# Kernel tuning notes

Hardware: AMD Instinct MI355X
Metric: run time of the kernel (lower is better)

The kernel has to match this reference:

```python
import jax, jax.numpy as jnp
import numpy as np

B, L, DM = 4, 409, 192            # batch, tokens (1 cls + 16 target + 196 template + 196 search), d_model
DI, DS, DR, K, DEPTH = 384, 16, 12, 4, 24   # d_inner=2*DM, d_state, dt_rank=ceil(DM/16), d_conv, depth
EPS = 1e-5


def setup_inputs() -> dict:
    key = jax.random.key(0)
    ks = list(jax.random.split(key, 16))
    def rn(i, shape, s=0.02):
        return jax.random.normal(ks[i], shape, jnp.float32) * s
    # S4D-real init: A = [1..d_state] per channel, stored as log
    A_log = jnp.log(jnp.tile(jnp.arange(1, DS + 1, dtype=jnp.float32), (DEPTH, DI, 1)))
    return {
        "tokens": jax.random.normal(ks[0], (B, L, DM), jnp.float32),
        "norm_w": jnp.ones((DEPTH, DM), jnp.float32),
        "in_proj_w": rn(1, (DEPTH, 2 * DI, DM)),
        "conv_w": rn(2, (DEPTH, DI, 1, K), 0.2),
        "conv_b": jnp.zeros((DEPTH, DI), jnp.float32),
        "conv_w_b": rn(3, (DEPTH, DI, 1, K), 0.2),
        "conv_b_b": jnp.zeros((DEPTH, DI), jnp.float32),
        "x_proj_w": rn(4, (DEPTH, DR + 2 * DS, DI)),
        "x_proj_w_b": rn(5, (DEPTH, DR + 2 * DS, DI)),
        "dt_proj_w": rn(6, (DEPTH, DI, DR), 0.1),
        "dt_bias": rn(7, (DEPTH, DI), 0.5),
        "dt_proj_w_b": rn(8, (DEPTH, DI, DR), 0.1),
        "dt_bias_b": rn(9, (DEPTH, DI), 0.5),
        "A_log": A_log,
        "A_log_b": A_log,
        "D_param": jnp.ones((DEPTH, DI), jnp.float32),
        "D_param_b": jnp.ones((DEPTH, DI), jnp.float32),
        "out_proj_w": rn(10, (DEPTH, DM, DI)),
        "norm_f_w": jnp.ones((DM,), jnp.float32),
    }


def _rms(x, w):
    return x * jax.lax.rsqrt(jnp.mean(x * x, -1, keepdims=True) + EPS) * w


def _causal_conv(x, w, b):
    # x [B,L,DI]; depthwise causal conv1d, kernel K (pad left K-1)
    y = jax.lax.conv_general_dilated(
        jnp.swapaxes(x, 1, 2), w, (1,), [(K - 1, 0)],
        dimension_numbers=("NCH", "OIH", "NCH"), feature_group_count=DI)
    return jnp.swapaxes(y + b[None, :, None], 1, 2)


def _selective_scan(u, delta, A, Bm, Cm, Dp):
    # u,delta [B,L,DI]; A [DI,DS]; Bm,Cm [B,L,DS]; Dp [DI]
    def step(h, inp):
        u_t, d_t, b_t, c_t = inp  # [B,DI],[B,DI],[B,DS],[B,DS]
        h = h * jnp.exp(d_t[..., None] * A) + (d_t * u_t)[..., None] * b_t[:, None, :]
        return h, jnp.einsum("bdn,bn->bd", h, c_t)
    h0 = jnp.zeros((u.shape[0], A.shape[0], A.shape[1]), u.dtype)
    xs = tuple(jnp.swapaxes(t, 0, 1) for t in (u, delta, Bm, Cm))
    _, ys = jax.lax.scan(step, h0, xs)
    return jnp.swapaxes(ys, 0, 1) + u * Dp


def _scan_dir(xin, cw, cb, xpw, dtw, dtb, a_log, dp):
    xf = jax.nn.silu(_causal_conv(xin, cw, cb))
    x_dbl = jnp.einsum("bld,ed->ble", xf, xpw)
    dt, Bm, Cm = jnp.split(x_dbl, [DR, DR + DS], axis=-1)
    dt = jax.nn.softplus(jnp.einsum("blr,dr->bld", dt, dtw) + dtb)
    return _selective_scan(xf, dt, -jnp.exp(a_log), Bm, Cm, dp)


def _mixer(x, p):
    # bimamba v2: forward scan + backward (flipped) scan with separate params
    xz = jnp.einsum("bld,ed->ble", x, p["in_proj_w"])
    xin, z = jnp.split(xz, 2, axis=-1)
    y_f = _scan_dir(xin, p["conv_w"], p["conv_b"], p["x_proj_w"],
                    p["dt_proj_w"], p["dt_bias"], p["A_log"], p["D_param"])
    y_b = _scan_dir(xin[:, ::-1], p["conv_w_b"], p["conv_b_b"], p["x_proj_w_b"],
                    p["dt_proj_w_b"], p["dt_bias_b"], p["A_log_b"], p["D_param_b"])[:, ::-1]
    y = (y_f + y_b) * jax.nn.silu(z) * 0.5   # z-gating + if_divide_out
    return jnp.einsum("ble,de->bld", y, p["out_proj_w"])


def reference(tokens, norm_w, in_proj_w, conv_w, conv_b, conv_w_b, conv_b_b,
              x_proj_w, x_proj_w_b, dt_proj_w, dt_bias, dt_proj_w_b, dt_bias_b,
              A_log, A_log_b, D_param, D_param_b, out_proj_w, norm_f_w):
    stacked = {"norm_w": norm_w, "in_proj_w": in_proj_w,
               "conv_w": conv_w, "conv_b": conv_b, "conv_w_b": conv_w_b, "conv_b_b": conv_b_b,
               "x_proj_w": x_proj_w, "x_proj_w_b": x_proj_w_b,
               "dt_proj_w": dt_proj_w, "dt_bias": dt_bias,
               "dt_proj_w_b": dt_proj_w_b, "dt_bias_b": dt_bias_b,
               "A_log": A_log, "A_log_b": A_log_b,
               "D_param": D_param, "D_param_b": D_param_b,
               "out_proj_w": out_proj_w}

    def layer(carry, p):
        hidden, residual = carry
        residual = residual + hidden          # add (first layer: residual starts at 0)
        h = _rms(residual, p["norm_w"])       # fused_add_norm prenorm path (RMSNorm)
        h = _mixer(h, p)
        return (h, residual), None

    init = (tokens, jnp.zeros_like(tokens))
    (hidden, residual), _ = jax.lax.scan(layer, init, stacked)
    return _rms(residual + hidden, norm_f_w)
```

## Files before the change

kernel.cpp:

```cpp
#include <hip/hip_runtime.h>
#include <math.h>

#define BB     4
#define LLEN   409
#define DMODEL 192
#define DINNER 384
#define DSTATE 16
#define DRANK  12
#define KCONV  4
#define NLAYER 24
#define NROW   (BB*LLEN)
#define EPSF   1e-5f
#define CH2    16
#define NCH2   26

__device__ __forceinline__ float siluf(float x){ return x/(1.f+__expf(-x)); }
__device__ __forceinline__ float softplusf(float x){ return (x>20.f)? x : log1pf(__expf(x)); }

__global__ void k_prep(const float* __restrict__ tokens, float* __restrict__ residual,
    const float* __restrict__ alF, const float* __restrict__ alB,
    float* __restrict__ anF, float* __restrict__ anB){
  int i = blockIdx.x*256+threadIdx.x;
  if (i < NROW*DMODEL) residual[i] = tokens[i];
  if (i < NLAYER*DINNER*DSTATE){
    int l = i/(DINNER*DSTATE); int rem = i%(DINNER*DSTATE);
    int nn = rem/DINNER, d = rem%DINNER;
    size_t src = ((size_t)l*DINNER + d)*DSTATE + nn;
    anF[i] = -expf(alF[src]);
    anB[i] = -expf(alB[src]);
  }
}

__global__ __launch_bounds__(256) void k_txp(const float* __restrict__ src,
    float* __restrict__ dst, int R, int C, int RP){
  __shared__ float t[32][33];
  int l = blockIdx.z;
  int c0 = blockIdx.x*32, r0 = blockIdx.y*32;
  const float* s = src + (size_t)l*R*C;
  float* d = dst + (size_t)l*C*RP;
  int tx = threadIdx.x, ty = threadIdx.y;
  #pragma unroll
  for (int yy=ty; yy<32; yy+=8){
    int rr = r0+yy, cc = c0+tx;
    t[yy][tx] = (rr<R && cc<C)? s[(size_t)rr*C+cc] : 0.f;
  }
  __syncthreads();
  #pragma unroll
  for (int yy=ty; yy<32; yy+=8){
    int cc = c0+yy, rr = r0+tx;
    if (cc<C && rr<RP) d[(size_t)cc*RP+rr] = t[tx][yy];
  }
}

__global__ __launch_bounds__(256) void k_prenorm(const float* __restrict__ residual,
    const float* __restrict__ norm_w, float* __restrict__ xn){
  int wv = threadIdx.x>>6, lane = threadIdx.x&63;
  int row = blockIdx.x*4 + wv;
  if (row >= NROW) return;
  float v[3]; float s = 0.f;
  #pragma unroll
  for (int q=0;q<3;q++){ v[q] = residual[(size_t)row*DMODEL + lane + q*64]; s += v[q]*v[q]; }
  #pragma unroll
  for (int off=1; off<64; off<<=1) s += __shfl_xor(s, off, 64);
  float sc = rsqrtf(s/(float)DMODEL + EPSF);
  #pragma unroll
  for (int q=0;q<3;q++) xn[(size_t)row*DMODEL + lane + q*64] = v[q]*sc*norm_w[lane + q*64];
}

__global__ __launch_bounds__(256) void k_gemm_in(const float* __restrict__ xn,
    const float* __restrict__ Wt, float* __restrict__ xz){
  __shared__ __align__(16) float w_lds[192*64];
  __shared__ __align__(16) float a_lds[192*20];
  int tid = threadIdx.x, r0 = blockIdx.x*16, c0 = blockIdx.y*64;
  {
    int j4 = (tid&15)*4, kr = tid>>4;
    #pragma unroll
    for (int s=0;s<12;s++){
      int k = kr + s*16;
      *reinterpret_cast<float4*>(&w_lds[k*64+j4]) =
        *reinterpret_cast<const float4*>(&Wt[(size_t)k*768 + c0 + j4]);
    }
  }
  {
    int i = tid>>4, kc = (tid&15)*12;
    int row = r0+i;
    #pragma unroll
    for (int m=0;m<12;m+=4){
      float4 v = make_float4(0.f,0.f,0.f,0.f);
      if (row<NROW) v = *reinterpret_cast<const float4*>(&xn[(size_t)row*192 + kc + m]);
      a_lds[(kc+m+0)*20+i]=v.x; a_lds[(kc+m+1)*20+i]=v.y;
      a_lds[(kc+m+2)*20+i]=v.z; a_lds[(kc+m+3)*20+i]=v.w;
    }
  }
  __syncthreads();
  int j = tid & 63, rg = tid >> 6;
  float acc[4] = {0.f,0.f,0.f,0.f};
  #pragma unroll 8
  for (int k=0;k<192;k++){
    float w = w_lds[k*64+j];
    float4 a = *reinterpret_cast<const float4*>(&a_lds[k*20 + rg*4]);
    acc[0]+=a.x*w; acc[1]+=a.y*w; acc[2]+=a.z*w; acc[3]+=a.w*w;
  }
  #pragma unroll
  for (int q=0;q<4;q++){
    int row = r0 + rg*4 + q;
    if (row<NROW) xz[(size_t)row*768 + c0 + j] = acc[q];
  }
}

__global__ __launch_bounds__(256) void k_conv(const float* __restrict__ xz,
    const float* __restrict__ cwf, const float* __restrict__ cbf,
    const float* __restrict__ cwb, const float* __restrict__ cbb,
    float* __restrict__ xf_f, float* __restrict__ xf_b){
  int idx = blockIdx.x*256 + threadIdx.x;
  if (idx >= NROW*(DINNER/4)) return;
  int d4 = (idx % (DINNER/4))*4; int bl = idx / (DINNER/4);
  int b = bl / LLEN; int l = bl % LLEN;
  int dir = blockIdx.y;
  const float* cw = dir? cwb : cwf;
  const float* cb = dir? cbb : cbf;
  float4 w0 = *reinterpret_cast<const float4*>(&cw[(d4+0)*KCONV]);
  float4 w1 = *reinterpret_cast<const float4*>(&cw[(d4+1)*KCONV]);
  float4 w2 = *reinterpret_cast<const float4*>(&cw[(d4+2)*KCONV]);
  float4 w3 = *reinterpret_cast<const float4*>(&cw[(d4+3)*KCONV]);
  float4 acc = *reinterpret_cast<const float4*>(&cb[d4]);
  const float* wa0 = (const float*)&w0; const float* wa1 = (const float*)&w1;
  const float* wa2 = (const float*)&w2; const float* wa3 = (const float*)&w3;
  #pragma unroll
  for (int k=0;k<KCONV;k++){
    int o = dir? (LLEN-1-l-k+3) : (l-3+k);
    bool ok = dir? (l+k>=3) : (o>=0);
    if (ok){
      float4 x = *reinterpret_cast<const float4*>(&xz[((size_t)(b*LLEN+o))*768 + d4]);
      acc.x += wa0[k]*x.x; acc.y += wa1[k]*x.y; acc.z += wa2[k]*x.z; acc.w += wa3[k]*x.w;
    }
  }
  float* out = dir? xf_b : xf_f;
  float4 r; r.x = siluf(acc.x); r.y = siluf(acc.y); r.z = siluf(acc.z); r.w = siluf(acc.w);
  *reinterpret_cast<float4*>(&out[(size_t)bl*DINNER + d4]) = r;
}

__global__ __launch_bounds__(256) void k_xp2(
    const float* __restrict__ xf_f, const float* __restrict__ xf_b,
    const float* __restrict__ WxpPF, const float* __restrict__ WxpPB,
    const float* __restrict__ WdtF, const float* __restrict__ WdtB,
    const float* __restrict__ dtbF, const float* __restrict__ dtbB,
    float* __restrict__ dtbc_f, float* __restrict__ dtbc_b,
    float* __restrict__ dt_f, float* __restrict__ dt_b){
  __shared__ __align__(16) float w_lds[192*64];
  __shared__ __align__(16) float a_lds[192*20];
  __shared__ float dtin_s[16*12];
  int dir = blockIdx.z;
  const float* xf  = dir? xf_b : xf_f;
  const float* Wxp = dir? WxpPB : WxpPF;
  const float* Wdt = dir? WdtB : WdtF;
  const float* dtb = dir? dtbB : dtbF;
  float* dtbc = dir? dtbc_b : dtbc_f;
  float* dtp  = dir? dt_b  : dt_f;
  int tid = threadIdx.x, r0 = blockIdx.x*16;
  int j = tid & 63, rg = tid >> 6;
  float acc[4] = {0.f,0.f,0.f,0.f};
  for (int c=0;c<2;c++){
    int K0 = c*192;
    if (c) __syncthreads();
    {
      int j4 = (tid&15)*4, kr = tid>>4;
      #pragma unroll
      for (int s=0;s<12;s++){
        int k = kr + s*16;
        *reinterpret_cast<float4*>(&w_lds[k*64+j4]) =
          *reinterpret_cast<const float4*>(&Wxp[(size_t)(K0+k)*64 + j4]);
      }
    }
    {
      int i = tid>>4, kc = (tid&15)*12;
      int row = r0+i;
      #pragma unroll
      for (int m=0;m<12;m+=4){
        float4 v = make_float4(0.f,0.f,0.f,0.f);
        if (row<NROW) v = *reinterpret_cast<const float4*>(&xf[(size_t)row*DINNER + K0 + kc + m]);
        a_lds[(kc+m+0)*20+i]=v.x; a_lds[(kc+m+1)*20+i]=v.y;
        a_lds[(kc+m+2)*20+i]=v.z; a_lds[(kc+m+3)*20+i]=v.w;
      }
    }
    __syncthreads();
    #pragma unroll 8
    for (int k=0;k<192;k++){
      float w = w_lds[k*64+j];
      float4 a = *reinterpret_cast<const float4*>(&a_lds[k*20 + rg*4]);
      acc[0]+=a.x*w; acc[1]+=a.y*w; acc[2]+=a.z*w; acc[3]+=a.w*w;
    }
  }
  __syncthreads();
  #pragma unroll
  for (int q=0;q<4;q++){
    int i = rg*4+q, row = r0+i;
    if (j<44 && row<NROW) dtbc[(size_t)row*44 + j] = acc[q];
    if (j<12) dtin_s[i*12 + j] = acc[q];
  }
  __syncthreads();
  for (int idx=tid; idx<12*DINNER; idx+=256) w_lds[idx] = Wdt[idx];
  __syncthreads();
  for (int idx=tid; idx<16*DINNER; idx+=256){
    int i = idx/DINNER, dd = idx - i*DINNER;
    int row = r0+i;
    float v = dtb[dd];
    #pragma unroll
    for (int r=0;r<12;r++) v += dtin_s[i*12+r]*w_lds[r*DINNER+dd];
    if (row<NROW) dtp[(size_t)row*DINNER+dd] = softplusf(v);
  }
}

__global__ __launch_bounds__(128) void k_scan1(
    const float* __restrict__ xf_f, const float* __restrict__ xf_b,
    const float* __restrict__ dtbc_f, const float* __restrict__ dtbc_b,
    const float* __restrict__ dt_f, const float* __restrict__ dt_b,
    const float* __restrict__ anF, const float* __restrict__ anB,
    float* __restrict__ q_buf, float* __restrict__ sdt_buf){
  int dir = blockIdx.z;
  int b  = blockIdx.y / NCH2;
  int ch = blockIdx.y % NCH2;
  if (ch == NCH2-1) return;
  const float* xf   = dir? xf_b  : xf_f;
  const float* dtbc = dir? dtbc_b: dtbc_f;
  const float* dtp  = dir? dt_b  : dt_f;
  const float* an   = dir? anB   : anF;
  int t0 = ch*CH2;
  int T  = CH2;
  int d0 = blockIdx.x*128;
  size_t base = (size_t)b*LLEN + t0;
  __shared__ float dt_s[CH2*128], u_s[CH2*128];
  __shared__ __align__(16) float B_s[CH2*16];
  int tid = threadIdx.x;
  for (int t=0;t<T;t++){
    dt_s[t*128+tid] = dtp[(base+t)*DINNER + d0 + tid];
    u_s [t*128+tid] = xf [(base+t)*DINNER + d0 + tid];
  }
  for (int idx = tid; idx < T*16; idx += 128){
    int t = idx>>4, n = idx&15;
    B_s[idx] = dtbc[(base+t)*44 + 12 + n];
  }
  __syncthreads();
  int d = d0 + tid;
  float A[16], h[16];
  #pragma unroll
  for (int n=0;n<16;n++){ A[n] = an[n*DINNER + d]; h[n] = 0.f; }
  float sdt = 0.f;
  for (int t=0;t<T;t++){
    float dtv = dt_s[t*128+tid];
    float du  = dtv * u_s[t*128+tid];
    float Bv[16];
    #pragma unroll
    for (int q=0;q<4;q++) *reinterpret_cast<float4*>(&Bv[q*4]) =
        *reinterpret_cast<const float4*>(&B_s[t*16 + q*4]);
    #pragma unroll
    for (int n=0;n<16;n++) h[n] = h[n]*__expf(dtv*A[n]) + du*Bv[n];
    sdt += dtv;
  }
  size_t ci = ((size_t)dir*BB + b)*NCH2 + ch;
  float* qo = &q_buf[(ci*DINNER + d)*DSTATE];
  #pragma unroll
  for (int q=0;q<4;q++) *reinterpret_cast<float4*>(&qo[q*4]) =
      make_float4(h[q*4+0], h[q*4+1], h[q*4+2], h[q*4+3]);
  sdt_buf[ci*DINNER + d] = sdt;
}

__global__ __launch_bounds__(128) void k_scan2(
    const float* __restrict__ xf_f, const float* __restrict__ xf_b,
    const float* __restrict__ dtbc_f, const float* __restrict__ dtbc_b,
    const float* __restrict__ dt_f, const float* __restrict__ dt_b,
    const float* __restrict__ anF, const float* __restrict__ anB,
    const float* __restrict__ DpF, const float* __restrict__ DpB,
    const float* __restrict__ q_buf, const float* __restrict__ sdt_buf,
    float* __restrict__ y_fo, float* __restrict__ y_bo){
  int dir = blockIdx.z;
  int b  = blockIdx.y / NCH2;
  int ch = blockIdx.y % NCH2;
  const float* xf   = dir? xf_b  : xf_f;
  const float* dtbc = dir? dtbc_b: dtbc_f;
  const float* dtp  = dir? dt_b  : dt_f;
  const float* an   = dir? anB   : anF;
  const float* Dp   = dir? DpB   : DpF;
  float* y = dir? y_bo : y_fo;
  int t0 = ch*CH2;
  int T  = (t0+CH2<=LLEN)? CH2 : (LLEN-t0);
  int d0 = blockIdx.x*128;
  size_t base = (size_t)b*LLEN + t0;
  __shared__ float dt_s[CH2*128], u_s[CH2*128];
  __shared__ __align__(16) float B_s[CH2*16], C_s[CH2*16];
  int tid = threadIdx.x;
  for (int t=0;t<T;t++){
    dt_s[t*128+tid] = dtp[(base+t)*DINNER + d0 + tid];
    u_s [t*128+tid] = xf [(base+t)*DINNER + d0 + tid];
  }
  for (int idx = tid; idx < T*16; idx += 128){
    int t = idx>>4, n = idx&15;
    B_s[idx] = dtbc[(base+t)*44 + 12 + n];
    C_s[idx] = dtbc[(base+t)*44 + 28 + n];
  }
  __syncthreads();
  int d = d0 + tid;
  float A[16], h[16];
  #pragma unroll
  for (int n=0;n<16;n++){ A[n] = an[n*DINNER + d]; h[n] = 0.f; }
  size_t sbase = ((size_t)dir*BB + b)*NCH2;
  for (int cc=0; cc<ch; cc++){
    float sv = sdt_buf[(sbase+cc)*DINNER + d];
    const float* qp = &q_buf[((sbase+cc)*DINNER + d)*DSTATE];
    float qv[16];
    #pragma unroll
    for (int q=0;q<4;q++) *reinterpret_cast<float4*>(&qv[q*4]) =
        *reinterpret_cast<const float4*>(&qp[q*4]);
    #pragma unroll
    for (int n=0;n<16;n++) h[n] = qv[n] + __expf(A[n]*sv)*h[n];
  }
  float Dd = Dp[d];
  for (int t=0;t<T;t++){
    float dtv = dt_s[t*128+tid];
    float u   = u_s [t*128+tid];
    float du  = dtv*u;
    float Bv[16], Cv[16];
    #pragma unroll
    for (int q=0;q<4;q++){
      *reinterpret_cast<float4*>(&Bv[q*4]) = *reinterpret_cast<const float4*>(&B_s[t*16+q*4]);
      *reinterpret_cast<float4*>(&Cv[q*4]) = *reinterpret_cast<const float4*>(&C_s[t*16+q*4]);
    }
    float y0=0.f, y1=0.f, y2=0.f, y3=0.f;
    #pragma unroll
    for (int n=0;n<16;n+=4){
      h[n+0] = h[n+0]*__expf(dtv*A[n+0]) + du*Bv[n+0];
      h[n+1] = h[n+1]*__expf(dtv*A[n+1]) + du*Bv[n+1];
      h[n+2] = h[n+2]*__expf(dtv*A[n+2]) + du*Bv[n+2];
      h[n+3] = h[n+3]*__expf(dtv*A[n+3]) + du*Bv[n+3];
      y0 += h[n+0]*Cv[n+0]; y1 += h[n+1]*Cv[n+1];
      y2 += h[n+2]*Cv[n+2]; y3 += h[n+3]*Cv[n+3];
    }
    y[(base+t)*DINNER + d] = (y0+y1)+(y2+y3) + u*Dd;
  }
}

__global__ __launch_bounds__(256) void k_gate(
    const float* __restrict__ y_f, const float* __restrict__ y_b,
    const float* __restrict__ xz, float* __restrict__ g){
  int idx = blockIdx.x*256 + threadIdx.x;
  if (idx >= NROW*(DINNER/4)) return;
  int d4 = (idx % (DINNER/4))*4; int row = idx / (DINNER/4);
  int b = row/LLEN, l = row%LLEN;
  int rrow = b*LLEN + (LLEN-1-l);
  float4 yf = *reinterpret_cast<const float4*>(&y_f[(size_t)row*DINNER + d4]);
  float4 yb = *reinterpret_cast<const float4*>(&y_b[(size_t)rrow*DINNER + d4]);
  float4 z  = *reinterpret_cast<const float4*>(&xz[(size_t)row*768 + DINNER + d4]);
  float4 r;
  r.x = (yf.x+yb.x)*siluf(z.x)*0.5f; r.y = (yf.y+yb.y)*siluf(z.y)*0.5f;
  r.z = (yf.z+yb.z)*siluf(z.z)*0.5f; r.w = (yf.w+yb.w)*siluf(z.w)*0.5f;
  *reinterpret_cast<float4*>(&g[(size_t)row*DINNER + d4]) = r;
}

__global__ __launch_bounds__(256) void k_gemm_out(const float* __restrict__ g,
    const float* __restrict__ Wt, float* __restrict__ residual){
  __shared__ __align__(16) float w_lds[192*64];
  __shared__ __align__(16) float a_lds[192*20];
  int tid = threadIdx.x, r0 = blockIdx.x*16, c0 = blockIdx.y*64;
  int j = tid & 63, rg = tid >> 6;
  float acc[4] = {0.f,0.f,0.f,0.f};
  for (int c=0;c<2;c++){
    int K0 = c*192;
    if (c) __syncthreads();
    {
      int j4 = (tid&15)*4, kr = tid>>4;
      #pragma unroll
      for (int s=0;s<12;s++){
        int k = kr + s*16;
        *reinterpret_cast<float4*>(&w_lds[k*64+j4]) =
          *reinterpret_cast<const float4*>(&Wt[(size_t)(K0+k)*192 + c0 + j4]);
      }
    }
    {
      int i = tid>>4, kc = (tid&15)*12;
      int row = r0+i;
      #pragma unroll
      for (int m=0;m<12;m+=4){
        float4 v = make_float4(0.f,0.f,0.f,0.f);
        if (row<NROW) v = *reinterpret_cast<const float4*>(&g[(size_t)row*DINNER + K0 + kc + m]);
        a_lds[(kc+m+0)*20+i]=v.x; a_lds[(kc+m+1)*20+i]=v.y;
        a_lds[(kc+m+2)*20+i]=v.z; a_lds[(kc+m+3)*20+i]=v.w;
      }
    }
    __syncthreads();
    #pragma unroll 8
    for (int k=0;k<192;k++){
      float w = w_lds[k*64+j];
      float4 a = *reinterpret_cast<const float4*>(&a_lds[k*20 + rg*4]);
      acc[0]+=a.x*w; acc[1]+=a.y*w; acc[2]+=a.z*w; acc[3]+=a.w*w;
    }
  }
  #pragma unroll
  for (int q=0;q<4;q++){
    int row = r0 + rg*4 + q;
    if (row<NROW) residual[(size_t)row*DMODEL + c0 + j] += acc[q];
  }
}

__global__ __launch_bounds__(256) void k_final(const float* __restrict__ residual,
    const float* __restrict__ nfw, float* __restrict__ out){
  int wv = threadIdx.x>>6, lane = threadIdx.x&63;
  int row = blockIdx.x*4 + wv;
  if (row >= NROW) return;
  float v[3]; float s = 0.f;
  #pragma unroll
  for (int q=0;q<3;q++){ v[q] = residual[(size_t)row*DMODEL + lane + q*64]; s += v[q]*v[q]; }
  #pragma unroll
  for (int off=1; off<64; off<<=1) s += __shfl_xor(s, off, 64);
  float sc = rsqrtf(s/(float)DMODEL + EPSF);
  #pragma unroll
  for (int q=0;q<3;q++) out[(size_t)row*DMODEL + lane + q*64] = v[q]*sc*nfw[lane + q*64];
}

extern "C" void kernel_launch(void* const* d_in, const int* in_sizes, int n_in,
                              void* d_out, int out_size, void* d_ws, size_t ws_size,
                              hipStream_t stream){
  const float* tokens     = (const float*)d_in[0];
  const float* norm_w     = (const float*)d_in[1];
  const float* in_proj_w  = (const float*)d_in[2];
  const float* conv_w     = (const float*)d_in[3];
  const float* conv_b     = (const float*)d_in[4];
  const float* conv_w_b   = (const float*)d_in[5];
  const float* conv_b_b   = (const float*)d_in[6];
  const float* x_proj_w   = (const float*)d_in[7];
  const float* x_proj_w_b = (const float*)d_in[8];
  const float* dt_proj_w  = (const float*)d_in[9];
  const float* dt_bias    = (const float*)d_in[10];
  const float* dt_proj_w_b= (const float*)d_in[11];
  const float* dt_bias_b  = (const float*)d_in[12];
  const float* A_log      = (const float*)d_in[13];
  const float* A_log_b    = (const float*)d_in[14];
  const float* D_param    = (const float*)d_in[15];
  const float* D_param_b  = (const float*)d_in[16];
  const float* out_proj_w = (const float*)d_in[17];
  const float* norm_f_w   = (const float*)d_in[18];

  float* ws = (float*)d_ws;
  size_t off = 0;
  float* residual = ws + off; off += (size_t)NROW*DMODEL;
  float* xn       = ws + off; off += (size_t)NROW*DMODEL;
  float* xz       = ws + off; off += (size_t)NROW*768;
  float* xf_f     = ws + off; off += (size_t)NROW*DINNER;
  float* xf_b     = ws + off; off += (size_t)NROW*DINNER;
  float* dtbc_f   = ws + off; off += (size_t)NROW*44;
  float* dtbc_b   = ws + off; off += (size_t)NROW*44;
  float* dt_f     = ws + off; off += (size_t)NROW*DINNER;
  float* dt_b     = ws + off; off += (size_t)NROW*DINNER;
  float* y_f      = ws + off; off += (size_t)NROW*DINNER;
  float* y_b      = ws + off; off += (size_t)NROW*DINNER;
  float* gbuf     = ws + off; off += (size_t)NROW*DINNER;
  float* q_buf    = ws + off; off += (size_t)2*BB*NCH2*DINNER*DSTATE;
  float* sdt_buf  = ws + off; off += (size_t)2*BB*NCH2*DINNER;
  float* WtIn     = ws + off; off += (size_t)NLAYER*DMODEL*768;
  float* WtXpPF   = ws + off; off += (size_t)NLAYER*DINNER*64;
  float* WtXpPB   = ws + off; off += (size_t)NLAYER*DINNER*64;
  float* WtDtF    = ws + off; off += (size_t)NLAYER*DRANK*DINNER;
  float* WtDtB    = ws + off; off += (size_t)NLAYER*DRANK*DINNER;
  float* WtOut    = ws + off; off += (size_t)NLAYER*DINNER*DMODEL;
  float* AnTF     = ws + off; off += (size_t)NLAYER*DINNER*DSTATE;
  float* AnTB     = ws + off; off += (size_t)NLAYER*DINNER*DSTATE;
  if (off*sizeof(float) > ws_size) return;

  k_prep<<<dim3((NROW*DMODEL+255)/256),256,0,stream>>>(tokens, residual, A_log, A_log_b, AnTF, AnTB);
  dim3 tb(32,8);
  k_txp<<<dim3(6,24,NLAYER),tb,0,stream>>>(in_proj_w,  WtIn,   768, 192, 768);
  k_txp<<<dim3(12,2,NLAYER),tb,0,stream>>>(x_proj_w,   WtXpPF,  44, 384,  64);
  k_txp<<<dim3(12,2,NLAYER),tb,0,stream>>>(x_proj_w_b, WtXpPB,  44, 384,  64);
  k_txp<<<dim3(1,12,NLAYER),tb,0,stream>>>(dt_proj_w,  WtDtF,  384,  12, 384);
  k_txp<<<dim3(1,12,NLAYER),tb,0,stream>>>(dt_proj_w_b,WtDtB,  384,  12, 384);
  k_txp<<<dim3(12,6,NLAYER),tb,0,stream>>>(out_proj_w, WtOut,  192, 384, 192);

  const int RT16 = (NROW+15)/16;
  const int EW4  = (NROW*(DINNER/4)+255)/256;
  for (int l=0; l<NLAYER; l++){
    k_prenorm<<<dim3((NROW+3)/4),256,0,stream>>>(residual, norm_w + (size_t)l*DMODEL, xn);
    k_gemm_in<<<dim3(RT16,12),256,0,stream>>>(xn, WtIn + (size_t)l*DMODEL*768, xz);
    k_conv<<<dim3(EW4,2),256,0,stream>>>(xz,
        conv_w + (size_t)l*DINNER*KCONV, conv_b + (size_t)l*DINNER,
        conv_w_b + (size_t)l*DINNER*KCONV, conv_b_b + (size_t)l*DINNER, xf_f, xf_b);
    k_xp2<<<dim3(RT16,1,2),256,0,stream>>>(xf_f, xf_b,
        WtXpPF + (size_t)l*DINNER*64, WtXpPB + (size_t)l*DINNER*64,
        WtDtF + (size_t)l*DRANK*DINNER, WtDtB + (size_t)l*DRANK*DINNER,
        dt_bias + (size_t)l*DINNER, dt_bias_b + (size_t)l*DINNER,
        dtbc_f, dtbc_b, dt_f, dt_b);
    k_scan1<<<dim3(3,BB*NCH2,2),128,0,stream>>>(xf_f, xf_b, dtbc_f, dtbc_b, dt_f, dt_b,
        AnTF + (size_t)l*DINNER*DSTATE, AnTB + (size_t)l*DINNER*DSTATE, q_buf, sdt_buf);
    k_scan2<<<dim3(3,BB*NCH2,2),128,0,stream>>>(xf_f, xf_b, dtbc_f, dtbc_b, dt_f, dt_b,
        AnTF + (size_t)l*DINNER*DSTATE, AnTB + (size_t)l*DINNER*DSTATE,
        D_param + (size_t)l*DINNER, D_param_b + (size_t)l*DINNER,
        q_buf, sdt_buf, y_f, y_b);
    k_gate<<<dim3(EW4),256,0,stream>>>(y_f, y_b, xz, gbuf);
    k_gemm_out<<<dim3(RT16,3),256,0,stream>>>(gbuf, WtOut + (size_t)l*DINNER*DMODEL, residual);
  }
  k_final<<<dim3((NROW+3)/4),256,0,stream>>>(residual, norm_f_w, (float*)d_out);
}
```

Measured before the change: 2.388 ms.

## Fuse forward/backward scan pass-2 with gating into one kernel

The second scan pass now handles both directions in one block. The block scans the forward chunk, keeps its outputs in LDS, then scans the matching range of the reversed sequence, which may straddle two backward chunks. It combines the two directions with the SiLU(z) gate and writes g directly. This removes the y_f/y_b global buffers and the separate gate kernel launch. In exchange the grid is halved, the two scans run serially in each block, LDS use is higher, and up to 25 backward steps are recomputed per block.

```diff
diff --git a/kernel.cpp b/kernel.cpp
--- a/kernel.cpp
+++ b/kernel.cpp
@@ -13,6 +13,7 @@
 #define EPSF   1e-5f
 #define CH2    16
 #define NCH2   26
+#define NSMAX  (CH2+9)
 
 __device__ __forceinline__ float siluf(float x){ return x/(1.f+__expf(-x)); }
 __device__ __forceinline__ float softplusf(float x){ return (x>20.f)? x : log1pf(__expf(x)); }
@@ -265,95 +266,145 @@
   sdt_buf[ci*DINNER + d] = sdt;
 }
 
-__global__ __launch_bounds__(128) void k_scan2(
+__global__ __launch_bounds__(128) void k_scan2g(
     const float* __restrict__ xf_f, const float* __restrict__ xf_b,
     const float* __restrict__ dtbc_f, const float* __restrict__ dtbc_b,
     const float* __restrict__ dt_f, const float* __restrict__ dt_b,
     const float* __restrict__ anF, const float* __restrict__ anB,
     const float* __restrict__ DpF, const float* __restrict__ DpB,
     const float* __restrict__ q_buf, const float* __restrict__ sdt_buf,
-    float* __restrict__ y_fo, float* __restrict__ y_bo){
-  int dir = blockIdx.z;
+    const float* __restrict__ xz, float* __restrict__ g){
   int b  = blockIdx.y / NCH2;
   int ch = blockIdx.y % NCH2;
-  const float* xf   = dir? xf_b  : xf_f;
-  const float* dtbc = dir? dtbc_b: dtbc_f;
-  const float* dtp  = dir? dt_b  : dt_f;
-  const float* an   = dir? anB   : anF;
-  const float* Dp   = dir? DpB   : DpF;
-  float* y = dir? y_bo : y_fo;
   int t0 = ch*CH2;
   int T  = (t0+CH2<=LLEN)? CH2 : (LLEN-t0);
   int d0 = blockIdx.x*128;
-  size_t base = (size_t)b*LLEN + t0;
-  __shared__ float dt_s[CH2*128], u_s[CH2*128];
-  __shared__ __align__(16) float B_s[CH2*16], C_s[CH2*16];
   int tid = threadIdx.x;
+  int d = d0 + tid;
+  size_t rbase = (size_t)b*LLEN;
+  int p_lo = LLEN - t0 - T;
+  int cb   = p_lo / CH2;
+  int bound= cb*CH2;
+  int pre  = p_lo - bound;
+  int ns   = (LLEN-1-t0) - bound + 1;
+
+  __shared__ float dtF_s[CH2*128], uF_s[CH2*128];
+  __shared__ float dtB_s[NSMAX*128], uB_s[NSMAX*128];
+  __shared__ __align__(16) float BF_s[CH2*16], CF_s[CH2*16];
+  __shared__ __align__(16) float BB_s[NSMAX*16], CB_s[NSMAX*16];
+  __shared__ float y_s[CH2*128];
+
   for (int t=0;t<T;t++){
-    dt_s[t*128+tid] = dtp[(base+t)*DINNER + d0 + tid];
-    u_s [t*128+tid] = xf [(base+t)*DINNER + d0 + tid];
-  }
-  for (int idx = tid; idx < T*16; idx += 128){
+    size_t r = rbase + t0 + t;
+    dtF_s[t*128+tid] = dt_f[r*DINNER + d];
+    uF_s [t*128+tid] = xf_f[r*DINNER + d];
+  }
+  for (int s=0;s<ns;s++){
+    size_t r = rbase + bound + s;
+    dtB_s[s*128+tid] = dt_b[r*DINNER + d];
+    uB_s [s*128+tid] = xf_b[r*DINNER + d];
+  }
+  for (int idx=tid; idx<T*16; idx+=128){
     int t = idx>>4, n = idx&15;
-    B_s[idx] = dtbc[(base+t)*44 + 12 + n];
-    C_s[idx] = dtbc[(base+t)*44 + 28 + n];
-  }
-  __syncthreads();
-  int d = d0 + tid;
-  float A[16], h[16];
-  #pragma unroll
-  for (int n=0;n<16;n++){ A[n] = an[n*DINNER + d]; h[n] = 0.f; }
-  size_t sbase = ((size_t)dir*BB + b)*NCH2;
-  for (int cc=0; cc<ch; cc++){
-    float sv = sdt_buf[(sbase+cc)*DINNER + d];
-    const float* qp = &q_buf[((sbase+cc)*DINNER + d)*DSTATE];
-    float qv[16];
-    #pragma unroll
-    for (int q=0;q<4;q++) *reinterpret_cast<float4*>(&qv[q*4]) =
-        *reinterpret_cast<const float4*>(&qp[q*4]);
-    #pragma unroll
-    for (int n=0;n<16;n++) h[n] = qv[n] + __expf(A[n]*sv)*h[n];
-  }
-  float Dd = Dp[d];
-  for (int t=0;t<T;t++){
-    float dtv = dt_s[t*128+tid];
-    float u   = u_s [t*128+tid];
-    float du  = dtv*u;
-    float Bv[16], Cv[16];
-    #pragma unroll
-    for (int q=0;q<4;q++){
-      *reinterpret_cast<float4*>(&Bv[q*4]) = *reinterpret_cast<const float4*>(&B_s[t*16+q*4]);
-      *reinterpret_cast<float4*>(&Cv[q*4]) = *reinterpret_cast<const float4*>(&C_s[t*16+q*4]);
-    }
-    float y0=0.f, y1=0.f, y2=0.f, y3=0.f;
-    #pragma unroll
-    for (int n=0;n<16;n+=4){
-      h[n+0] = h[n+0]*__expf(dtv*A[n+0]) + du*Bv[n+0];
-      h[n+1] = h[n+1]*__expf(dtv*A[n+1]) + du*Bv[n+1];
-      h[n+2] = h[n+2]*__expf(dtv*A[n+2]) + du*Bv[n+2];
-      h[n+3] = h[n+3]*__expf(dtv*A[n+3]) + du*Bv[n+3];
-      y0 += h[n+0]*Cv[n+0]; y1 += h[n+1]*Cv[n+1];
-      y2 += h[n+2]*Cv[n+2]; y3 += h[n+3]*Cv[n+3];
-    }
-    y[(base+t)*DINNER + d] = (y0+y1)+(y2+y3) + u*Dd;
-  }
-}
-
-__global__ __launch_bounds__(256) void k_gate(
-    const float* __restrict__ y_f, const float* __restrict__ y_b,
-    const float* __restrict__ xz, float* __restrict__ g){
-  int idx = blockIdx.x*256 + threadIdx.x;
-  if (idx >= NROW*(DINNER/4)) return;
-  int d4 = (idx % (DINNER/4))*4; int row = idx / (DINNER/4);
-  int b = row/LLEN, l = row%LLEN;
-  int rrow = b*LLEN + (LLEN-1-l);
-  float4 yf = *reinterpret_cast<const float4*>(&y_f[(size_t)row*DINNER + d4]);
-  float4 yb = *reinterpret_cast<const float4*>(&y_b[(size_t)rrow*DINNER + d4]);
-  float4 z  = *reinterpret_cast<const float4*>(&xz[(size_t)row*768 + DINNER + d4]);
-  float4 r;
-  r.x = (yf.x+yb.x)*siluf(z.x)*0.5f; r.y = (yf.y+yb.y)*siluf(z.y)*0.5f;
-  r.z = (yf.z+yb.z)*siluf(z.z)*0.5f; r.w = (yf.w+yb.w)*siluf(z.w)*0.5f;
-  *reinterpret_cast<float4*>(&g[(size_t)row*DINNER + d4]) = r;
+    size_t r = rbase + t0 + t;
+    BF_s[idx] = dtbc_f[r*44 + 12 + n];
+    CF_s[idx] = dtbc_f[r*44 + 28 + n];
+  }
+  for (int idx=tid; idx<ns*16; idx+=128){
+    int s = idx>>4, n = idx&15;
+    size_t r = rbase + bound + s;
+    BB_s[idx] = dtbc_b[r*44 + 12 + n];
+    CB_s[idx] = dtbc_b[r*44 + 28 + n];
+  }
+  __syncthreads();
+
+  {
+    float A[16], h[16];
+    #pragma unroll
+    for (int n=0;n<16;n++){ A[n] = anF[n*DINNER + d]; h[n] = 0.f; }
+    size_t sb = (size_t)b*NCH2;
+    for (int cc=0; cc<ch; cc++){
+      float sv = sdt_buf[(sb+cc)*DINNER + d];
+      const float* qp = &q_buf[((sb+cc)*DINNER + d)*DSTATE];
+      float qv[16];
+      #pragma unroll
+      for (int q=0;q<4;q++) *reinterpret_cast<float4*>(&qv[q*4]) =
+          *reinterpret_cast<const float4*>(&qp[q*4]);
+      #pragma unroll
+      for (int n=0;n<16;n++) h[n] = qv[n] + __expf(A[n]*sv)*h[n];
+    }
+    float Dd = DpF[d];
+    for (int t=0;t<T;t++){
+      float dtv = dtF_s[t*128+tid];
+      float u   = uF_s [t*128+tid];
+      float du  = dtv*u;
+      float Bv[16], Cv[16];
+      #pragma unroll
+      for (int q=0;q<4;q++){
+        *reinterpret_cast<float4*>(&Bv[q*4]) = *reinterpret_cast<const float4*>(&BF_s[t*16+q*4]);
+        *reinterpret_cast<float4*>(&Cv[q*4]) = *reinterpret_cast<const float4*>(&CF_s[t*16+q*4]);
+      }
+      float y0=0.f, y1=0.f, y2=0.f, y3=0.f;
+      #pragma unroll
+      for (int n=0;n<16;n+=4){
+        h[n+0] = h[n+0]*__expf(dtv*A[n+0]) + du*Bv[n+0];
+        h[n+1] = h[n+1]*__expf(dtv*A[n+1]) + du*Bv[n+1];
+        h[n+2] = h[n+2]*__expf(dtv*A[n+2]) + du*Bv[n+2];
+        h[n+3] = h[n+3]*__expf(dtv*A[n+3]) + du*Bv[n+3];
+        y0 += h[n+0]*Cv[n+0]; y1 += h[n+1]*Cv[n+1];
+        y2 += h[n+2]*Cv[n+2]; y3 += h[n+3]*Cv[n+3];
+      }
+      y_s[t*128+tid] = (y0+y1)+(y2+y3) + u*Dd;
+    }
+  }
+
+  {
+    float A[16], h[16];
+    #pragma unroll
+    for (int n=0;n<16;n++){ A[n] = anB[n*DINNER + d]; h[n] = 0.f; }
+    size_t sb = ((size_t)BB + b)*NCH2;
+    for (int cc=0; cc<cb; cc++){
+      float sv = sdt_buf[(sb+cc)*DINNER + d];
+      const float* qp = &q_buf[((sb+cc)*DINNER + d)*DSTATE];
+      float qv[16];
+      #pragma unroll
+      for (int q=0;q<4;q++) *reinterpret_cast<float4*>(&qv[q*4]) =
+          *reinterpret_cast<const float4*>(&qp[q*4]);
+      #pragma unroll
+      for (int n=0;n<16;n++) h[n] = qv[n] + __expf(A[n]*sv)*h[n];
+    }
+    float Dd = DpB[d];
+    for (int s=0;s<ns;s++){
+      float dtv = dtB_s[s*128+tid];
+      float u   = uB_s [s*128+tid];
+      float du  = dtv*u;
+      float Bv[16], Cv[16];
+      #pragma unroll
+      for (int q=0;q<4;q++){
+        *reinterpret_cast<float4*>(&Bv[q*4]) = *reinterpret_cast<const float4*>(&BB_s[s*16+q*4]);
+        *reinterpret_cast<float4*>(&Cv[q*4]) = *reinterpret_cast<const float4*>(&CB_s[s*16+q*4]);
+      }
+      float y0=0.f, y1=0.f, y2=0.f, y3=0.f;
+      #pragma unroll
+      for (int n=0;n<16;n+=4){
+        h[n+0] = h[n+0]*__expf(dtv*A[n+0]) + du*Bv[n+0];
+        h[n+1] = h[n+1]*__expf(dtv*A[n+1]) + du*Bv[n+1];
+        h[n+2] = h[n+2]*__expf(dtv*A[n+2]) + du*Bv[n+2];
+        h[n+3] = h[n+3]*__expf(dtv*A[n+3]) + du*Bv[n+3];
+        y0 += h[n+0]*Cv[n+0]; y1 += h[n+1]*Cv[n+1];
+        y2 += h[n+2]*Cv[n+2]; y3 += h[n+3]*Cv[n+3];
+      }
+      if (s >= pre){
+        int p = bound + s;
+        int l = LLEN-1-p;
+        int t = l - t0;
+        size_t row = rbase + l;
+        float yb = (y0+y1)+(y2+y3) + u*Dd;
+        float z  = xz[row*768 + DINNER + d];
+        g[row*DINNER + d] = (y_s[t*128+tid] + yb)*siluf(z)*0.5f;
+      }
+    }
+  }
 }
 
 __global__ __launch_bounds__(256) void k_gemm_out(const float* __restrict__ g,
@@ -450,8 +501,6 @@
   float* dtbc_b   = ws + off; off += (size_t)NROW*44;
   float* dt_f     = ws + off; off += (size_t)NROW*DINNER;
   float* dt_b     = ws + off; off += (size_t)NROW*DINNER;
-  float* y_f      = ws + off; off += (size_t)NROW*DINNER;
-  float* y_b      = ws + off; off += (size_t)NROW*DINNER;
   float* gbuf     = ws + off; off += (size_t)NROW*DINNER;
   float* q_buf    = ws + off; off += (size_t)2*BB*NCH2*DINNER*DSTATE;
   float* sdt_buf  = ws + off; off += (size_t)2*BB*NCH2*DINNER;
@@ -489,11 +538,10 @@
         dtbc_f, dtbc_b, dt_f, dt_b);
     k_scan1<<<dim3(3,BB*NCH2,2),128,0,stream>>>(xf_f, xf_b, dtbc_f, dtbc_b, dt_f, dt_b,
         AnTF + (size_t)l*DINNER*DSTATE, AnTB + (size_t)l*DINNER*DSTATE, q_buf, sdt_buf);
-    k_scan2<<<dim3(3,BB*NCH2,2),128,0,stream>>>(xf_f, xf_b, dtbc_f, dtbc_b, dt_f, dt_b,
+    k_scan2g<<<dim3(3,BB*NCH2),128,0,stream>>>(xf_f, xf_b, dtbc_f, dtbc_b, dt_f, dt_b,
         AnTF + (size_t)l*DINNER*DSTATE, AnTB + (size_t)l*DINNER*DSTATE,
         D_param + (size_t)l*DINNER, D_param_b + (size_t)l*DINNER,
-        q_buf, sdt_buf, y_f, y_b);
-    k_gate<<<dim3(EW4),256,0,stream>>>(y_f, y_b, xz, gbuf);
+        q_buf, sdt_buf, xz, gbuf);
     k_gemm_out<<<dim3(RT16,3),256,0,stream>>>(gbuf, WtOut + (size_t)l*DINNER*DMODEL, residual);
   }
   k_final<<<dim3((NROW+3)/4),256,0,stream>>>(residual, norm_f_w, (float*)d_out);
```

Measured after the change: 2.694 ms. +12.8%, slower.
